# Optimization experiments

Measured on AMD Instinct MI355X. Metric: run time of the kernel, lower is better.

## Reference

```python
import jax, jax.numpy as jnp
import numpy as np

N_ANGLES = 180
N_DETECTORS = 256


def _bilinear_sample(img, x, y):
    """Bilinear sample img[y, x]; zero outside. img: [H, W]; x, y: any shape."""
    H, W = img.shape
    x0 = jnp.floor(x)
    y0 = jnp.floor(y)
    xi = x0.astype(jnp.int32)
    yi = y0.astype(jnp.int32)
    wx = x - x0
    wy = y - y0

    def get(ix, iy):
        valid = (ix >= 0) & (ix < W) & (iy >= 0) & (iy < H)
        ixc = jnp.clip(ix, 0, W - 1)
        iyc = jnp.clip(iy, 0, H - 1)
        return jnp.where(valid, img[iyc, ixc], jnp.zeros((), img.dtype))

    v00 = get(xi, yi)
    v01 = get(xi + 1, yi)
    v10 = get(xi, yi + 1)
    v11 = get(xi + 1, yi + 1)
    return (v00 * (1.0 - wx) + v01 * wx) * (1.0 - wy) + (v10 * (1.0 - wx) + v11 * wx) * wy


def setup_inputs() -> dict:
    key = jax.random.key(0)
    inputs = jax.random.uniform(key, (8, 256, 256, 1), dtype=jnp.float32)
    return {"inputs": inputs}


def reference(inputs):
    # Parallel-beam forward Radon transform (forwardproject).
    # inputs: [B, H, W, 1] image batch -> sinogram [B, n_angles, n_detectors, 1]
    B, H, W, _ = inputs.shape
    A, D = N_ANGLES, N_DETECTORS
    T = H  # integration samples along each ray

    theta = jnp.linspace(0.0, jnp.pi, A, endpoint=False, dtype=inputs.dtype)
    cos_t = jnp.cos(theta)[:, None, None]  # [A,1,1]
    sin_t = jnp.sin(theta)[:, None, None]

    s = (jnp.arange(D, dtype=inputs.dtype) - (D - 1) / 2.0)[None, :, None]  # detector offsets
    t = (jnp.arange(T, dtype=inputs.dtype) - (T - 1) / 2.0)[None, None, :]  # along-ray offsets

    cx = (W - 1) / 2.0
    cy = (H - 1) / 2.0
    # sample coords for every (angle, detector, ray-step): [A, D, T]
    x = cx + s * cos_t - t * sin_t
    y = cy + s * sin_t + t * cos_t

    imgs = inputs[..., 0]  # [B, H, W]
    vals = jax.vmap(lambda im: _bilinear_sample(im, x, y))(imgs)  # [B, A, D, T]
    sino = vals.sum(axis=-1)  # ray integral (unit step length)
    return sino[..., None]  # [B, A, D, 1]
```

## Files before the change

### kernel.cpp

```cpp
#include <hip/hip_runtime.h>
#include <math.h>

#define NA    180
#define HB    9
#define KB    29
#define P0C   261
#define P0R   273
#define TROWS 12
#define TSZ   (P0C * TROWS)
#define OUTN  (8 * NA * 256)

typedef _Float16 h2  __attribute__((ext_vector_type(2)));
typedef _Float16 h8  __attribute__((ext_vector_type(8)));
typedef __fp16   hf2 __attribute__((ext_vector_type(2)));

__device__ __forceinline__ h2 pkrtz(float a, float b) {
    hf2 t = __builtin_amdgcn_cvt_pkrtz(a, b);
    return __builtin_bit_cast(h2, t);
}
__device__ __forceinline__ float fdot2f(h2 a, h2 b, float c) {
#if __has_builtin(__builtin_amdgcn_fdot2)
    return __builtin_amdgcn_fdot2(__builtin_bit_cast(hf2, a),
                                  __builtin_bit_cast(hf2, b), c, false);
#else
    return c + (float)a.x * (float)b.x + (float)a.y * (float)b.y;
#endif
}
__device__ __forceinline__ float imc(const float* im, int y, int x) {
    return ((unsigned)y < 256u && (unsigned)x < 256u) ? im[(y << 8) + x] : 0.0f;
}

__global__ __launch_bounds__(256) void prep_kernel(
    const float* __restrict__ img, uint4* __restrict__ P0,
    uint4* __restrict__ P1, float* __restrict__ out, float* __restrict__ tab)
{
    const int tid = threadIdx.x;
    const int row = blockIdx.x;
    const int mb  = blockIdx.y;

    if (mb == 0) {
        for (int i = row * 256 + tid; i < OUTN; i += P0R * 256) out[i] = 0.0f;
    }
    if (mb == 1 && row == 0 && tid < NA) {
        const float theta = (float)tid * ((float)M_PI / (float)NA);
        tab[tid]      = cosf(theta);
        tab[tid + NA] = sinf(theta);
    }

    const int bg = mb & 1;
    const float* im0 = img + ((size_t)(bg * 4) << 16);
    const int v = row - 4;

    if (mb < 2) {
        uint4* dst = P0 + (size_t)(bg * P0R + row) * P0C;
        for (int j = tid; j < P0C; j += 256) {
            const int u = j - 2;
            h8 t;
            t[0] = (_Float16)imc(im0,             v, u); t[1] = (_Float16)imc(im0,             v + 1, u);
            t[2] = (_Float16)imc(im0 + (1 << 16), v, u); t[3] = (_Float16)imc(im0 + (1 << 16), v + 1, u);
            t[4] = (_Float16)imc(im0 + (2 << 16), v, u); t[5] = (_Float16)imc(im0 + (2 << 16), v + 1, u);
            t[6] = (_Float16)imc(im0 + (3 << 16), v, u); t[7] = (_Float16)imc(im0 + (3 << 16), v + 1, u);
            dst[j] = __builtin_bit_cast(uint4, t);
        }
    } else {
        uint4* dst = P1 + (size_t)(bg * P0R + row) * P0C;
        for (int j = tid; j < P0C; j += 256) {
            const int u = j - 2;
            h8 t;
            t[0] = (_Float16)imc(im0,             u, v); t[1] = (_Float16)imc(im0,             u, v + 1);
            t[2] = (_Float16)imc(im0 + (1 << 16), u, v); t[3] = (_Float16)imc(im0 + (1 << 16), u, v + 1);
            t[4] = (_Float16)imc(im0 + (2 << 16), u, v); t[5] = (_Float16)imc(im0 + (2 << 16), u, v + 1);
            t[6] = (_Float16)imc(im0 + (3 << 16), u, v); t[7] = (_Float16)imc(im0 + (3 << 16), u, v + 1);
            dst[j] = __builtin_bit_cast(uint4, t);
        }
    }
}

#define SAMPLE(JV, UV, VPV, A0, A1, A2, A3)                                   \
    {                                                                         \
        const float ucl = fminf(fmaxf((UV), -1.5f), 257.5f);                  \
        const float uf = floorf(ucl);                                         \
        const float wu = ucl - uf;                                            \
        const float vf = floorf(VPV);                                         \
        const float wv = (VPV) - vf;                                          \
        const float vfc = fminf(fmaxf(vf, -2.0f), 9.0f);                      \
        const int idx = (int)fmaf(vfc, 261.0f, uf) + 524;                     \
        const h8 A8 = __builtin_bit_cast(h8, s_tile[idx]);                    \
        const h8 B8 = __builtin_bit_cast(h8, s_tile[idx + 1]);                \
        const h2 wu2 = pkrtz(wu, wu);                                         \
        const h8 wu8 = __builtin_shufflevector(wu2, wu2, 0,1,0,1,0,1,0,1);    \
        const h8 tb8 = (B8 - A8) * wu8 + A8;                                  \
        h2 wv2 = pkrtz(1.0f - wv, wv);                                        \
        wv2 = ((unsigned)(JV) < span) ? wv2 : hz;                             \
        A0 = fdot2f(__builtin_shufflevector(tb8, tb8, 0, 1), wv2, A0);        \
        A1 = fdot2f(__builtin_shufflevector(tb8, tb8, 2, 3), wv2, A1);        \
        A2 = fdot2f(__builtin_shufflevector(tb8, tb8, 4, 5), wv2, A2);        \
        A3 = fdot2f(__builtin_shufflevector(tb8, tb8, 6, 7), wv2, A3);        \
    }

template<bool MODEX>
__device__ __forceinline__ void radon_body(
    const uint4* __restrict__ Pbase,
    float* __restrict__ out, const float* __restrict__ tab,
    uint4* s_tile, int tid, int b0, int p, int gi)
{
    const int lo = -2 + p * HB;

    {
        const uint4* src = Pbase + (size_t)(lo + 2) * P0C;
        for (int i = tid; i < TSZ; i += 256) s_tile[i] = src[i];
    }
    __syncthreads();

    const float detf = (float)tid - 127.5f;
    const float lof = (float)lo;
    const h2 hz = {};

    for (int g = 0; g < 7; ++g) {
        const int ai = gi * 7 + g;
        int a;
        if (MODEX) { if (ai >= 89) break; a = 46 + ai; }
        else       { a = (ai <= 45) ? ai : 89 + ai; }

        const float c = tab[a];
        const float s = tab[a + NA];

        const float xc = 127.5f + detf * c + 127.5f * s;
        const float yc = 127.5f + detf * s - 127.5f * c;

        const float ucst = MODEX ? yc : xc;
        const float vcst = MODEX ? xc : yc;
        const float du   = MODEX ? c  : -s;
        const float dv   = MODEX ? -s : c;

        const float inv = 1.0f / dv;
        const float f1 = (lof - vcst) * inv;
        const float f2 = (lof + (float)HB - vcst) * inv;
        const float fmn = fminf(f1, f2);
        const float fmx = fmaxf(f1, f2);
        int kmin, kend;
        if (dv > 0.0f) { kmin = (int)ceilf(fmn);      kend = (int)ceilf(fmx); }
        else           { kmin = (int)floorf(fmn) + 1; kend = (int)floorf(fmx) + 1; }

        const int len = kend - kmin;
        const int jlo = max(0, -kmin);
        const int jhi = min(len, 256 - kmin);
        const int spani = max(0, jhi - jlo);
        if (!__any(spani > 0)) continue;
        const unsigned span = (unsigned)spani;

        const int kstart = kmin + jlo;
        const int Lmax = (int)((float)HB * fabsf(inv)) + 2;

        float u  = fmaf((float)kstart, du, ucst);
        float vp = fmaf((float)kstart, dv, vcst - lof);
        const float du2 = du + du, dv2 = dv + dv;

        float a0 = 0.f, a1 = 0.f, a2 = 0.f, a3 = 0.f;
        float b0a = 0.f, b1a = 0.f, b2a = 0.f, b3a = 0.f;

        int j = 0;
        for (; j + 1 < Lmax; j += 2) {
            SAMPLE(j,     u,      vp,      a0, a1, a2, a3);
            SAMPLE(j + 1, u + du, vp + dv, b0a, b1a, b2a, b3a);
            u += du2; vp += dv2;
        }
        if (j < Lmax) SAMPLE(j, u, vp, a0, a1, a2, a3);

        if (spani > 0) {
            float* o = &out[((b0 * NA + a) << 8) + tid];
            atomicAdd(o,                 a0 + b0a);
            atomicAdd(o + (NA << 8),     a1 + b1a);
            atomicAdd(o + 2 * (NA << 8), a2 + b2a);
            atomicAdd(o + 3 * (NA << 8), a3 + b3a);
        }
    }
}

__global__ __launch_bounds__(256, 3) void radon_kernel(
    const uint4* __restrict__ P0, const uint4* __restrict__ P1,
    float* __restrict__ out, const float* __restrict__ tab)
{
    __shared__ uint4 s_tile[TSZ];
    const int tid = threadIdx.x;
    const int bg  = blockIdx.x;
    const int p   = blockIdx.y;
    const int gid = blockIdx.z;
    const int b0  = bg * 4;
    if (gid < 13)
        radon_body<false>(P0 + (size_t)bg * P0R * P0C, out, tab, s_tile, tid, b0, p, gid);
    else
        radon_body<true>(P1 + (size_t)bg * P0R * P0C, out, tab, s_tile, tid, b0, p, gid - 13);
}

extern "C" void kernel_launch(void* const* d_in, const int* in_sizes, int n_in,
                              void* d_out, int out_size, void* d_ws, size_t ws_size,
                              hipStream_t stream) {
    const float* img = (const float*)d_in[0];
    float* out = (float*)d_out;

    uint4* P0 = (uint4*)d_ws;
    uint4* P1 = P0 + (size_t)2 * P0R * P0C;
    float* tab = (float*)(P1 + (size_t)2 * P0R * P0C);

    prep_kernel<<<dim3(P0R, 4), 256, 0, stream>>>(img, P0, P1, out, tab);
    radon_kernel<<<dim3(2, KB, 26), 256, 0, stream>>>(P0, P1, out, tab);
}
```

Measured before the change: 111.6 us.

## Store single-row fp16 tiles and do 4-tap bilinear from LDS

The prepacked tile changes from 8 halves per texel (two rows times four images) to 4 halves (one row times four images), which halves the LDS tile footprint. The sample loop now reads four 8-byte LDS entries, interpolates along v first and then does the u-weighted dot product. With the smaller shared memory, launch bounds go from 3 to 6 blocks per CU to raise occupancy. The trade is twice as many LDS loads per sample, plus different padding and row offsets in the prepacked buffers.

```diff
diff --git a/kernel.cpp b/kernel.cpp
--- a/kernel.cpp
+++ b/kernel.cpp
@@ -4,14 +4,15 @@
 #define NA    180
 #define HB    9
 #define KB    29
-#define P0C   261
-#define P0R   273
+#define PC    262
+#define PR    264
 #define TROWS 12
-#define TSZ   (P0C * TROWS)
+#define TSZ   (PC * TROWS)
+#define TSZ4  (TSZ / 2)
 #define OUTN  (8 * NA * 256)
 
 typedef _Float16 h2  __attribute__((ext_vector_type(2)));
-typedef _Float16 h8  __attribute__((ext_vector_type(8)));
+typedef _Float16 h4  __attribute__((ext_vector_type(4)));
 typedef __fp16   hf2 __attribute__((ext_vector_type(2)));
 
 __device__ __forceinline__ h2 pkrtz(float a, float b) {
@@ -31,15 +32,15 @@
 }
 
 __global__ __launch_bounds__(256) void prep_kernel(
-    const float* __restrict__ img, uint4* __restrict__ P0,
-    uint4* __restrict__ P1, float* __restrict__ out, float* __restrict__ tab)
+    const float* __restrict__ img, uint2* __restrict__ P0,
+    uint2* __restrict__ P1, float* __restrict__ out, float* __restrict__ tab)
 {
     const int tid = threadIdx.x;
     const int row = blockIdx.x;
     const int mb  = blockIdx.y;
 
     if (mb == 0) {
-        for (int i = row * 256 + tid; i < OUTN; i += P0R * 256) out[i] = 0.0f;
+        for (int i = row * 256 + tid; i < OUTN; i += PR * 256) out[i] = 0.0f;
     }
     if (mb == 1 && row == 0 && tid < NA) {
         const float theta = (float)tid * ((float)M_PI / (float)NA);
@@ -49,29 +50,33 @@
 
     const int bg = mb & 1;
     const float* im0 = img + ((size_t)(bg * 4) << 16);
-    const int v = row - 4;
+    const int v = row - 3;
 
     if (mb < 2) {
-        uint4* dst = P0 + (size_t)(bg * P0R + row) * P0C;
-        for (int j = tid; j < P0C; j += 256) {
+        uint2* dst = P0 + (size_t)(bg * PR + row) * PC;
+        for (int j = tid; j < PC; j += 256) {
             const int u = j - 2;
-            h8 t;
-            t[0] = (_Float16)imc(im0,             v, u); t[1] = (_Float16)imc(im0,             v + 1, u);
-            t[2] = (_Float16)imc(im0 + (1 << 16), v, u); t[3] = (_Float16)imc(im0 + (1 << 16), v + 1, u);
-            t[4] = (_Float16)imc(im0 + (2 << 16), v, u); t[5] = (_Float16)imc(im0 + (2 << 16), v + 1, u);
-            t[6] = (_Float16)imc(im0 + (3 << 16), v, u); t[7] = (_Float16)imc(im0 + (3 << 16), v + 1, u);
-            dst[j] = __builtin_bit_cast(uint4, t);
+            h4 t = {};
+            if (j < 261) {
+                t[0] = (_Float16)imc(im0,             v, u);
+                t[1] = (_Float16)imc(im0 + (1 << 16), v, u);
+                t[2] = (_Float16)imc(im0 + (2 << 16), v, u);
+                t[3] = (_Float16)imc(im0 + (3 << 16), v, u);
+            }
+            dst[j] = __builtin_bit_cast(uint2, t);
         }
     } else {
-        uint4* dst = P1 + (size_t)(bg * P0R + row) * P0C;
-        for (int j = tid; j < P0C; j += 256) {
+        uint2* dst = P1 + (size_t)(bg * PR + row) * PC;
+        for (int j = tid; j < PC; j += 256) {
             const int u = j - 2;
-            h8 t;
-            t[0] = (_Float16)imc(im0,             u, v); t[1] = (_Float16)imc(im0,             u, v + 1);
-            t[2] = (_Float16)imc(im0 + (1 << 16), u, v); t[3] = (_Float16)imc(im0 + (1 << 16), u, v + 1);
-            t[4] = (_Float16)imc(im0 + (2 << 16), u, v); t[5] = (_Float16)imc(im0 + (2 << 16), u, v + 1);
-            t[6] = (_Float16)imc(im0 + (3 << 16), u, v); t[7] = (_Float16)imc(im0 + (3 << 16), u, v + 1);
-            dst[j] = __builtin_bit_cast(uint4, t);
+            h4 t = {};
+            if (j < 261) {
+                t[0] = (_Float16)imc(im0,             u, v);
+                t[1] = (_Float16)imc(im0 + (1 << 16), u, v);
+                t[2] = (_Float16)imc(im0 + (2 << 16), u, v);
+                t[3] = (_Float16)imc(im0 + (3 << 16), u, v);
+            }
+            dst[j] = __builtin_bit_cast(uint2, t);
         }
     }
 }
@@ -83,32 +88,36 @@
         const float wu = ucl - uf;                                            \
         const float vf = floorf(VPV);                                         \
         const float wv = (VPV) - vf;                                          \
-        const float vfc = fminf(fmaxf(vf, -2.0f), 9.0f);                      \
-        const int idx = (int)fmaf(vfc, 261.0f, uf) + 524;                     \
-        const h8 A8 = __builtin_bit_cast(h8, s_tile[idx]);                    \
-        const h8 B8 = __builtin_bit_cast(h8, s_tile[idx + 1]);                \
-        const h2 wu2 = pkrtz(wu, wu);                                         \
-        const h8 wu8 = __builtin_shufflevector(wu2, wu2, 0,1,0,1,0,1,0,1);    \
-        const h8 tb8 = (B8 - A8) * wu8 + A8;                                  \
-        h2 wv2 = pkrtz(1.0f - wv, wv);                                        \
-        wv2 = ((unsigned)(JV) < span) ? wv2 : hz;                             \
-        A0 = fdot2f(__builtin_shufflevector(tb8, tb8, 0, 1), wv2, A0);        \
-        A1 = fdot2f(__builtin_shufflevector(tb8, tb8, 2, 3), wv2, A1);        \
-        A2 = fdot2f(__builtin_shufflevector(tb8, tb8, 4, 5), wv2, A2);        \
-        A3 = fdot2f(__builtin_shufflevector(tb8, tb8, 6, 7), wv2, A3);        \
+        const float vfc = fminf(fmaxf(vf, -1.0f), 9.0f);                      \
+        const int idx = (int)fmaf(vfc, (float)PC, uf) + (PC + 2);             \
+        const h4 r00 = __builtin_bit_cast(h4, s_tile[idx]);                   \
+        const h4 r01 = __builtin_bit_cast(h4, s_tile[idx + 1]);               \
+        const h4 r10 = __builtin_bit_cast(h4, s_tile[idx + PC]);              \
+        const h4 r11 = __builtin_bit_cast(h4, s_tile[idx + PC + 1]);          \
+        const h2 wv2 = pkrtz(wv, wv);                                         \
+        const h4 wv4 = __builtin_shufflevector(wv2, wv2, 0, 1, 0, 1);         \
+        const h4 V0 = (r10 - r00) * wv4 + r00;                                \
+        const h4 V1 = (r11 - r01) * wv4 + r01;                                \
+        h2 wu2 = pkrtz(1.0f - wu, wu);                                        \
+        wu2 = ((unsigned)(JV) < span) ? wu2 : hz;                             \
+        A0 = fdot2f(__builtin_shufflevector(V0, V1, 0, 4), wu2, A0);          \
+        A1 = fdot2f(__builtin_shufflevector(V0, V1, 1, 5), wu2, A1);          \
+        A2 = fdot2f(__builtin_shufflevector(V0, V1, 2, 6), wu2, A2);          \
+        A3 = fdot2f(__builtin_shufflevector(V0, V1, 3, 7), wu2, A3);          \
     }
 
 template<bool MODEX>
 __device__ __forceinline__ void radon_body(
-    const uint4* __restrict__ Pbase,
+    const uint2* __restrict__ Pbase,
     float* __restrict__ out, const float* __restrict__ tab,
-    uint4* s_tile, int tid, int b0, int p, int gi)
+    uint2* s_tile, int tid, int b0, int p, int gi)
 {
     const int lo = -2 + p * HB;
 
     {
-        const uint4* src = Pbase + (size_t)(lo + 2) * P0C;
-        for (int i = tid; i < TSZ; i += 256) s_tile[i] = src[i];
+        const uint4* src = (const uint4*)(Pbase + (size_t)(lo + 2) * PC);
+        uint4* dst = (uint4*)s_tile;
+        for (int i = tid; i < TSZ4; i += 256) dst[i] = src[i];
     }
     __syncthreads();
 
@@ -177,20 +186,20 @@
     }
 }
 
-__global__ __launch_bounds__(256, 3) void radon_kernel(
-    const uint4* __restrict__ P0, const uint4* __restrict__ P1,
+__global__ __launch_bounds__(256, 6) void radon_kernel(
+    const uint2* __restrict__ P0, const uint2* __restrict__ P1,
     float* __restrict__ out, const float* __restrict__ tab)
 {
-    __shared__ uint4 s_tile[TSZ];
+    __shared__ uint2 s_tile[TSZ];
     const int tid = threadIdx.x;
     const int bg  = blockIdx.x;
     const int p   = blockIdx.y;
     const int gid = blockIdx.z;
     const int b0  = bg * 4;
     if (gid < 13)
-        radon_body<false>(P0 + (size_t)bg * P0R * P0C, out, tab, s_tile, tid, b0, p, gid);
+        radon_body<false>(P0 + (size_t)bg * PR * PC, out, tab, s_tile, tid, b0, p, gid);
     else
-        radon_body<true>(P1 + (size_t)bg * P0R * P0C, out, tab, s_tile, tid, b0, p, gid - 13);
+        radon_body<true>(P1 + (size_t)bg * PR * PC, out, tab, s_tile, tid, b0, p, gid - 13);
 }
 
 extern "C" void kernel_launch(void* const* d_in, const int* in_sizes, int n_in,
@@ -199,10 +208,10 @@
     const float* img = (const float*)d_in[0];
     float* out = (float*)d_out;
 
-    uint4* P0 = (uint4*)d_ws;
-    uint4* P1 = P0 + (size_t)2 * P0R * P0C;
-    float* tab = (float*)(P1 + (size_t)2 * P0R * P0C);
-
-    prep_kernel<<<dim3(P0R, 4), 256, 0, stream>>>(img, P0, P1, out, tab);
+    uint2* P0 = (uint2*)d_ws;
+    uint2* P1 = P0 + (size_t)2 * PR * PC;
+    float* tab = (float*)(P1 + (size_t)2 * PR * PC);
+
+    prep_kernel<<<dim3(PR, 4), 256, 0, stream>>>(img, P0, P1, out, tab);
     radon_kernel<<<dim3(2, KB, 26), 256, 0, stream>>>(P0, P1, out, tab);
 }
```

New measurement: 106.2 us. 1.05x faster.

## Shrink angle groups, trim padded tile rows, and unroll ray loop by four

Applied to the files above, without the earlier changes.

Angles per block drop from 7 to 4, so the grid grows from 26 to 46 groups in z and there are more blocks with shorter serial work. The padded plane trims one halo row (272 down to 263 rows, 11 tile rows) and widens rows to 262 columns, which shrinks the shared tile and allows more resident blocks. The inner sampling loop is unrolled by four with independent accumulators to expose more memory-level parallelism. In exchange, each block reloads its tile for fewer angles, adds more atomics per block, and uses more registers.

```diff
diff --git a/kernel.cpp b/kernel.cpp
--- a/kernel.cpp
+++ b/kernel.cpp
@@ -4,11 +4,13 @@
 #define NA    180
 #define HB    9
 #define KB    29
-#define P0C   261
-#define P0R   273
-#define TROWS 12
-#define TSZ   (P0C * TROWS)
+#define PC    262
+#define PR    263
+#define TROWS 11
+#define TSZ   (PC * TROWS)
 #define OUTN  (8 * NA * 256)
+#define APG   4
+#define NG    23
 
 typedef _Float16 h2  __attribute__((ext_vector_type(2)));
 typedef _Float16 h8  __attribute__((ext_vector_type(8)));
@@ -39,7 +41,7 @@
     const int mb  = blockIdx.y;
 
     if (mb == 0) {
-        for (int i = row * 256 + tid; i < OUTN; i += P0R * 256) out[i] = 0.0f;
+        for (int i = row * 256 + tid; i < OUTN; i += PR * 256) out[i] = 0.0f;
     }
     if (mb == 1 && row == 0 && tid < NA) {
         const float theta = (float)tid * ((float)M_PI / (float)NA);
@@ -49,28 +51,32 @@
 
     const int bg = mb & 1;
     const float* im0 = img + ((size_t)(bg * 4) << 16);
-    const int v = row - 4;
+    const int v = row - 3;
 
     if (mb < 2) {
-        uint4* dst = P0 + (size_t)(bg * P0R + row) * P0C;
-        for (int j = tid; j < P0C; j += 256) {
+        uint4* dst = P0 + (size_t)(bg * PR + row) * PC;
+        for (int j = tid; j < PC; j += 256) {
             const int u = j - 2;
-            h8 t;
-            t[0] = (_Float16)imc(im0,             v, u); t[1] = (_Float16)imc(im0,             v + 1, u);
-            t[2] = (_Float16)imc(im0 + (1 << 16), v, u); t[3] = (_Float16)imc(im0 + (1 << 16), v + 1, u);
-            t[4] = (_Float16)imc(im0 + (2 << 16), v, u); t[5] = (_Float16)imc(im0 + (2 << 16), v + 1, u);
-            t[6] = (_Float16)imc(im0 + (3 << 16), v, u); t[7] = (_Float16)imc(im0 + (3 << 16), v + 1, u);
+            h8 t = {};
+            if (j < 261) {
+                t[0] = (_Float16)imc(im0,             v, u); t[1] = (_Float16)imc(im0,             v + 1, u);
+                t[2] = (_Float16)imc(im0 + (1 << 16), v, u); t[3] = (_Float16)imc(im0 + (1 << 16), v + 1, u);
+                t[4] = (_Float16)imc(im0 + (2 << 16), v, u); t[5] = (_Float16)imc(im0 + (2 << 16), v + 1, u);
+                t[6] = (_Float16)imc(im0 + (3 << 16), v, u); t[7] = (_Float16)imc(im0 + (3 << 16), v + 1, u);
+            }
             dst[j] = __builtin_bit_cast(uint4, t);
         }
     } else {
-        uint4* dst = P1 + (size_t)(bg * P0R + row) * P0C;
-        for (int j = tid; j < P0C; j += 256) {
+        uint4* dst = P1 + (size_t)(bg * PR + row) * PC;
+        for (int j = tid; j < PC; j += 256) {
             const int u = j - 2;
-            h8 t;
-            t[0] = (_Float16)imc(im0,             u, v); t[1] = (_Float16)imc(im0,             u, v + 1);
-            t[2] = (_Float16)imc(im0 + (1 << 16), u, v); t[3] = (_Float16)imc(im0 + (1 << 16), u, v + 1);
-            t[4] = (_Float16)imc(im0 + (2 << 16), u, v); t[5] = (_Float16)imc(im0 + (2 << 16), u, v + 1);
-            t[6] = (_Float16)imc(im0 + (3 << 16), u, v); t[7] = (_Float16)imc(im0 + (3 << 16), u, v + 1);
+            h8 t = {};
+            if (j < 261) {
+                t[0] = (_Float16)imc(im0,             u, v); t[1] = (_Float16)imc(im0,             u, v + 1);
+                t[2] = (_Float16)imc(im0 + (1 << 16), u, v); t[3] = (_Float16)imc(im0 + (1 << 16), u, v + 1);
+                t[4] = (_Float16)imc(im0 + (2 << 16), u, v); t[5] = (_Float16)imc(im0 + (2 << 16), u, v + 1);
+                t[6] = (_Float16)imc(im0 + (3 << 16), u, v); t[7] = (_Float16)imc(im0 + (3 << 16), u, v + 1);
+            }
             dst[j] = __builtin_bit_cast(uint4, t);
         }
     }
@@ -83,8 +89,8 @@
         const float wu = ucl - uf;                                            \
         const float vf = floorf(VPV);                                         \
         const float wv = (VPV) - vf;                                          \
-        const float vfc = fminf(fmaxf(vf, -2.0f), 9.0f);                      \
-        const int idx = (int)fmaf(vfc, 261.0f, uf) + 524;                     \
+        const float vfc = fminf(fmaxf(vf, -1.0f), 9.0f);                      \
+        const int idx = (int)fmaf(vfc, (float)PC, uf) + (PC + 2);             \
         const h8 A8 = __builtin_bit_cast(h8, s_tile[idx]);                    \
         const h8 B8 = __builtin_bit_cast(h8, s_tile[idx + 1]);                \
         const h2 wu2 = pkrtz(wu, wu);                                         \
@@ -107,7 +113,7 @@
     const int lo = -2 + p * HB;
 
     {
-        const uint4* src = Pbase + (size_t)(lo + 2) * P0C;
+        const uint4* src = Pbase + (size_t)(lo + 2) * PC;
         for (int i = tid; i < TSZ; i += 256) s_tile[i] = src[i];
     }
     __syncthreads();
@@ -116,11 +122,11 @@
     const float lof = (float)lo;
     const h2 hz = {};
 
-    for (int g = 0; g < 7; ++g) {
-        const int ai = gi * 7 + g;
+    for (int g = 0; g < APG; ++g) {
+        const int ai = gi * APG + g;
         int a;
         if (MODEX) { if (ai >= 89) break; a = 46 + ai; }
-        else       { a = (ai <= 45) ? ai : 89 + ai; }
+        else       { if (ai >= 91) break; a = (ai <= 45) ? ai : 89 + ai; }
 
         const float c = tab[a];
         const float s = tab[a + NA];
@@ -155,24 +161,35 @@
         float u  = fmaf((float)kstart, du, ucst);
         float vp = fmaf((float)kstart, dv, vcst - lof);
         const float du2 = du + du, dv2 = dv + dv;
+        const float du3 = du2 + du, dv3 = dv2 + dv;
+        const float du4 = du2 + du2, dv4 = dv2 + dv2;
 
         float a0 = 0.f, a1 = 0.f, a2 = 0.f, a3 = 0.f;
-        float b0a = 0.f, b1a = 0.f, b2a = 0.f, b3a = 0.f;
+        float e0 = 0.f, e1 = 0.f, e2 = 0.f, e3 = 0.f;
+        float c0 = 0.f, c1 = 0.f, c2 = 0.f, c3 = 0.f;
+        float d0 = 0.f, d1 = 0.f, d2 = 0.f, d3 = 0.f;
 
         int j = 0;
+        for (; j + 3 < Lmax; j += 4) {
+            SAMPLE(j,     u,        vp,        a0, a1, a2, a3);
+            SAMPLE(j + 1, u + du,   vp + dv,   e0, e1, e2, e3);
+            SAMPLE(j + 2, u + du2,  vp + dv2,  c0, c1, c2, c3);
+            SAMPLE(j + 3, u + du3,  vp + dv3,  d0, d1, d2, d3);
+            u += du4; vp += dv4;
+        }
         for (; j + 1 < Lmax; j += 2) {
             SAMPLE(j,     u,      vp,      a0, a1, a2, a3);
-            SAMPLE(j + 1, u + du, vp + dv, b0a, b1a, b2a, b3a);
+            SAMPLE(j + 1, u + du, vp + dv, e0, e1, e2, e3);
             u += du2; vp += dv2;
         }
         if (j < Lmax) SAMPLE(j, u, vp, a0, a1, a2, a3);
 
         if (spani > 0) {
             float* o = &out[((b0 * NA + a) << 8) + tid];
-            atomicAdd(o,                 a0 + b0a);
-            atomicAdd(o + (NA << 8),     a1 + b1a);
-            atomicAdd(o + 2 * (NA << 8), a2 + b2a);
-            atomicAdd(o + 3 * (NA << 8), a3 + b3a);
+            atomicAdd(o,                 (a0 + c0) + (e0 + d0));
+            atomicAdd(o + (NA << 8),     (a1 + c1) + (e1 + d1));
+            atomicAdd(o + 2 * (NA << 8), (a2 + c2) + (e2 + d2));
+            atomicAdd(o + 3 * (NA << 8), (a3 + c3) + (e3 + d3));
         }
     }
 }
@@ -187,10 +204,10 @@
     const int p   = blockIdx.y;
     const int gid = blockIdx.z;
     const int b0  = bg * 4;
-    if (gid < 13)
-        radon_body<false>(P0 + (size_t)bg * P0R * P0C, out, tab, s_tile, tid, b0, p, gid);
+    if (gid < NG)
+        radon_body<false>(P0 + (size_t)bg * PR * PC, out, tab, s_tile, tid, b0, p, gid);
     else
-        radon_body<true>(P1 + (size_t)bg * P0R * P0C, out, tab, s_tile, tid, b0, p, gid - 13);
+        radon_body<true>(P1 + (size_t)bg * PR * PC, out, tab, s_tile, tid, b0, p, gid - NG);
 }
 
 extern "C" void kernel_launch(void* const* d_in, const int* in_sizes, int n_in,
@@ -200,9 +217,9 @@
     float* out = (float*)d_out;
 
     uint4* P0 = (uint4*)d_ws;
-    uint4* P1 = P0 + (size_t)2 * P0R * P0C;
-    float* tab = (float*)(P1 + (size_t)2 * P0R * P0C);
-
-    prep_kernel<<<dim3(P0R, 4), 256, 0, stream>>>(img, P0, P1, out, tab);
-    radon_kernel<<<dim3(2, KB, 26), 256, 0, stream>>>(P0, P1, out, tab);
-}
+    uint4* P1 = P0 + (size_t)2 * PR * PC;
+    float* tab = (float*)(P1 + (size_t)2 * PR * PC);
+
+    prep_kernel<<<dim3(PR, 4), 256, 0, stream>>>(img, P0, P1, out, tab);
+    radon_kernel<<<dim3(2, KB, 2 * NG), 256, 0, stream>>>(P0, P1, out, tab);
+}
```

Result: no change. 112.2 us (+0.6%).
